# Kernel optimization log

Measured on AMD Instinct MI355X. Metric: run time of the kernel, lower is better.

The kernel has to match this reference:

```python
import jax
import jax.numpy as jnp
import numpy as np
from jax import lax

DELTA = float(np.exp(-2.0))  # rule-creation density threshold


def codebook_lamb(x):
    """Online growing RBF prototype codebook (ALMMo-style) for one layer.

    x: [N, M]. Returns lamb: [N] normalized density of each sample at its
    assigned rule. Faithful (corrected) semantics of Layer.__call__:
      - SEN = squared L2 norm per sample (over feature dim)
      - global mean / mean squared norm over the batch
      - sequential per-sample: if max RBF density over existing rules < exp(-2),
        append a new rule (prototype=c=x, SENc=||x||^2, support=1);
        else update rule_star. Note the source's `support[rule_star] = +1`
        assigns 1, so the running mean update degenerates to c[rule_star]=x,
        SENc[rule_star]=||x||^2 -- replicated here.
      - distances use the (never-updated) prototypes; bandwidth stau uses c.
    """
    N, M = x.shape
    SENx = jnp.sum(x * x, axis=-1)                      # [N]
    gmean = jnp.mean(x, axis=0)                         # [M]
    base = jnp.mean(SENx) - jnp.sum(gmean * gmean)      # SENgmean - SEN(gmean)
    R = N                                               # worst case: one rule/sample

    protos0 = jnp.zeros((R, M), x.dtype)
    pn20 = jnp.zeros((R,), x.dtype)                     # ||proto_r||^2 (carried)
    c0 = jnp.zeros((R, M), x.dtype)
    cn20 = jnp.zeros((R,), x.dtype)                     # ||c_r||^2 (carried)
    SENc0 = jnp.zeros((R,), x.dtype)
    count0 = jnp.int32(0)

    ridx = jnp.arange(R)

    def step(carry, inp):
        protos, pn2, c, cn2, SENc, count = carry
        xi, sxi = inp                                   # [M], scalar
        valid = ridx < count
        stau = (base + SENc - cn2) * 0.5                # [R]
        dist = sxi + pn2 - 2.0 * (protos @ xi)          # [R] ||xi - proto_r||^2
        dens = jnp.where(valid, jnp.exp(-dist / stau), -jnp.inf)
        idx = jnp.argmax(dens)
        vmax = dens[idx]
        new = (count == 0) | (vmax < DELTA)
        slot = jnp.where(new, count, idx)
        # both branches set c/SENc at slot to xi/sxi (support resets to 1)
        c = c.at[slot].set(xi)
        cn2 = cn2.at[slot].set(sxi)
        SENc = SENc.at[slot].set(sxi)
        # only a new rule writes a prototype (OOB scatter when count==R is dropped)
        protos = protos.at[count].set(jnp.where(new, xi, protos[count]))
        pn2 = pn2.at[count].set(jnp.where(new, sxi, pn2[count]))
        count = count + new.astype(count.dtype)
        return (protos, pn2, c, cn2, SENc, count), slot

    (protos, pn2, c, cn2, SENc, count), rules = lax.scan(
        step, (protos0, pn20, c0, cn20, SENc0, count0), (x, SENx)
    )

    # final densities of all samples under all (valid) rules: [R, N]
    stau = (base + SENc - cn2) * 0.5                    # [R]
    dist = SENx[None, :] + pn2[:, None] - 2.0 * (protos @ x.T)
    dens = jnp.where((ridx < count)[:, None], jnp.exp(-dist / stau[:, None]), 0.0)
    dens_xn = dens[rules, jnp.arange(N)]                # density at assigned rule
    lamb = dens_xn / jnp.sum(dens, axis=0)              # normalize over rules
    return lamb


def setup_inputs() -> dict:
    key = jax.random.key(0)
    k = jax.random.split(key, 5)
    N, D_IN, D_H, D_OUT = 2048, 2048, 2048, 1024
    s0 = 1.0 / np.sqrt(D_IN)
    s1 = 1.0 / np.sqrt(D_H)
    return {
        "x": jax.random.normal(k[0], (N, D_IN), jnp.float32),
        "W0": jax.random.normal(k[1], (D_H, D_IN), jnp.float32) * s0,
        "b0": jax.random.normal(k[2], (D_H,), jnp.float32) * s0,
        "W1": jax.random.normal(k[3], (D_OUT, D_H), jnp.float32) * s1,
        "b1": jax.random.normal(k[4], (D_OUT,), jnp.float32) * s1,
    }


def reference(x, W0, b0, W1, b1):
    lambs = []
    h = x
    for W, b in ((W0, b0), (W1, b1)):
        lambs.append(codebook_lamb(h))          # per-layer codebook on layer input
        h = jax.nn.sigmoid(h @ W.T + b)         # torch.nn.Linear + sigmoid
    return h, jnp.stack(lambs)                  # ([N, d_out], [n_layers, N])
```

## Files before the change

### kernel.cpp

```cpp
#include <hip/hip_runtime.h>
#include <cstdint>
#include <cstddef>


#define DELTA_F 0.13533528323661270f
#define MBYTE (1u << 20)

typedef __bf16 bf16;
typedef bf16 bf16x8 __attribute__((ext_vector_type(8)));
typedef bf16 bf16x4 __attribute__((ext_vector_type(4)));
typedef float f32x4 __attribute__((ext_vector_type(4)));

typedef __attribute__((address_space(1))) void as1_void;
typedef __attribute__((address_space(3))) void as3_void;

__device__ __forceinline__ void gload16(const bf16* g, bf16* l) {
  __builtin_amdgcn_global_load_lds((as1_void*)g, (as3_void*)l, 16, 0, 0);
}

template <bool IS_L0>
__global__ __launch_bounds__(512, 4) void gemm_fused(
    const bf16* __restrict__ A, float* __restrict__ Dens,
    bf16* __restrict__ Hb, float* __restrict__ Fo,
    const float* __restrict__ bias, const float* __restrict__ SENin,
    const float* __restrict__ ninv_p, float* __restrict__ S,
    int* __restrict__ e, float* __restrict__ SENhOut,
    float* __restrict__ colsumH) {
  __shared__ __align__(16) char smem[32768];
  const int tid = threadIdx.x;
  const int wave = tid >> 6, lane = tid & 63;
  const int quad = lane >> 4, l16 = lane & 15;
  const int kg = wave & 1, wm = (wave >> 1) & 1, wn = (wave >> 2) & 1;
  const int m0 = blockIdx.y * 128, n0 = blockIdx.x * 128;
  const int waveM = wm * 64, waveN = wn * 64;
  const bool isGram = (n0 < 2048);
  const int sr8 = lane >> 3, slot = lane & 7;
  const int gk = (slot ^ sr8) * 8;
  const bf16* aSrc = A + (size_t)(m0 + wave * 16 + sr8) * 2048 + gk;
  const bf16* bSrc = A + (size_t)(n0 + wave * 16 + sr8) * 2048 + gk;
  char* const aDst = smem + wave * 2048;
  char* const bDst = smem + 16384 + wave * 2048;
  const int swz = ((kg * 4 + quad) ^ (l16 & 7)) * 16;
  const int aOff = (waveM + l16) * 128 + swz;
  const int bOff = 16384 + (waveN + l16) * 128 + swz;

  f32x4 acc[4][4] = {};
  for (int k0 = 0; k0 < 2048; k0 += 64) {
    gload16(aSrc + k0, (bf16*)aDst);
    gload16(aSrc + 8 * 2048 + k0, (bf16*)(aDst + 1024));
    gload16(bSrc + k0, (bf16*)bDst);
    gload16(bSrc + 8 * 2048 + k0, (bf16*)(bDst + 1024));
    __syncthreads();
    bf16x8 af[4], bfr[4];
#pragma unroll
    for (int i = 0; i < 4; ++i) af[i] = *(const bf16x8*)(smem + aOff + i * 2048);
#pragma unroll
    for (int j = 0; j < 4; ++j) bfr[j] = *(const bf16x8*)(smem + bOff + j * 2048);
#pragma unroll
    for (int i = 0; i < 4; ++i)
#pragma unroll
      for (int j = 0; j < 4; ++j)
        acc[i][j] = __builtin_amdgcn_mfma_f32_16x16x32_bf16(af[i], bfr[j], acc[i][j], 0, 0, 0);
    __syncthreads();
  }

  const float ninv = ninv_p[0];
  float colp[4] = {0.f, 0.f, 0.f, 0.f};
  char* const ex = smem + (wn * 2 + wm) * 8192;
#pragma unroll
  for (int round = 0; round < 2; ++round) {
    __syncthreads();
    if (kg == 1) {
#pragma unroll
      for (int ii = 0; ii < 2; ++ii)
#pragma unroll
        for (int j = 0; j < 4; ++j)
          *(f32x4*)(ex + (ii * 4 + j) * 1024 + lane * 16) = acc[round * 2 + ii][j];
    }
    __syncthreads();
    if (kg == 0) {
#pragma unroll
      for (int ii = 0; ii < 2; ++ii) {
        const int i = round * 2 + ii;
        const int rbase = m0 + waveM + i * 16 + quad * 4;
        if (isGram) {
          const f32x4 si4 = *(const f32x4*)(SENin + rbase);
          float rp[4] = {0.f, 0.f, 0.f, 0.f};
          int er = 0;
#pragma unroll
          for (int j = 0; j < 4; ++j) {
            f32x4 v = acc[i][j] + *(const f32x4*)(ex + (ii * 4 + j) * 1024 + lane * 16);
            const int col = n0 + waveN + j * 16 + l16;
            const float sj = SENin[col];
#pragma unroll
            for (int r = 0; r < 4; ++r) {
              const float dens = __expf((si4[r] + sj - 2.0f * v[r]) * ninv);
              Dens[(size_t)(rbase + r) * 2048 + col] = dens;
              rp[r] += dens;
              if (col < rbase + r && dens >= DELTA_F) er |= (1 << r);
            }
          }
#pragma unroll
          for (int r = 0; r < 4; ++r) {
            float rv = rp[r];
            rv += __shfl_xor(rv, 1, 64); rv += __shfl_xor(rv, 2, 64);
            rv += __shfl_xor(rv, 4, 64); rv += __shfl_xor(rv, 8, 64);
            if (l16 == 0) atomicAdd(S + rbase + r, rv);
          }
          er |= __shfl_xor(er, 1, 64); er |= __shfl_xor(er, 2, 64);
          er |= __shfl_xor(er, 4, 64); er |= __shfl_xor(er, 8, 64);
          if (l16 == 0 && er) {
#pragma unroll
            for (int r = 0; r < 4; ++r)
              if ((er >> r) & 1) atomicOr(e + rbase + r, 1);
          }
        } else {
          float rn[4] = {0.f, 0.f, 0.f, 0.f};
#pragma unroll
          for (int j = 0; j < 4; ++j) {
            f32x4 v = acc[i][j] + *(const f32x4*)(ex + (ii * 4 + j) * 1024 + lane * 16);
            const int c2 = n0 - 2048 + waveN + j * 16 + l16;
            const float bv = bias[c2];
#pragma unroll
            for (int r = 0; r < 4; ++r) {
              const float hv = 1.0f / (1.0f + __expf(-(v[r] + bv)));
              if (IS_L0) {
                Hb[(size_t)(rbase + r) * 2048 + c2] = (bf16)hv;
                rn[r] += hv * hv;
                colp[j] += hv;
              } else {
                Fo[(size_t)(rbase + r) * 1024 + c2] = hv;
              }
            }
          }
          if (IS_L0) {
#pragma unroll
            for (int r = 0; r < 4; ++r) {
              float rv = rn[r];
              rv += __shfl_xor(rv, 1, 64); rv += __shfl_xor(rv, 2, 64);
              rv += __shfl_xor(rv, 4, 64); rv += __shfl_xor(rv, 8, 64);
              if (l16 == 0) atomicAdd(SENhOut + rbase + r, rv);
            }
          }
        }
      }
    }
  }
  if (IS_L0 && !isGram && kg == 0) {
#pragma unroll
    for (int j = 0; j < 4; ++j) {
      float cv = colp[j];
      cv += __shfl_xor(cv, 16, 64);
      cv += __shfl_xor(cv, 32, 64);
      if (lane < 16) atomicAdd(colsumH + (n0 - 2048 + waveN + j * 16 + lane), cv);
    }
  }
}

__device__ __forceinline__ float wave_reduce(float s) {
  for (int o = 32; o > 0; o >>= 1) s += __shfl_down(s, o, 64);
  return s;
}

__global__ void f2b_all(const float* __restrict__ x, const float* __restrict__ W0,
                        const float* __restrict__ W1, bf16* __restrict__ xb,
                        bf16* __restrict__ wb0, bf16* __restrict__ wb1,
                        float* __restrict__ SENx, float* __restrict__ cpartX) {
  const int b = blockIdx.x, tid = threadIdx.x;
  const int wave = tid >> 6, lane = tid & 63;
  if (b < 256) {
    const int r0 = b * 8;
    __shared__ float ws[8][4];
    f32x4 c0 = {0.f, 0.f, 0.f, 0.f}, c1 = {0.f, 0.f, 0.f, 0.f};
    for (int r = 0; r < 8; ++r) {
      const float* src = x + (size_t)(r0 + r) * 2048;
      bf16* dst = xb + (size_t)(r0 + r) * 2048;
      f32x4 v0 = *(const f32x4*)(src + tid * 4);
      f32x4 v1 = *(const f32x4*)(src + 1024 + tid * 4);
      bf16x4 o0, o1;
      o0.x = (bf16)v0.x; o0.y = (bf16)v0.y; o0.z = (bf16)v0.z; o0.w = (bf16)v0.w;
      o1.x = (bf16)v1.x; o1.y = (bf16)v1.y; o1.z = (bf16)v1.z; o1.w = (bf16)v1.w;
      *(bf16x4*)(dst + tid * 4) = o0;
      *(bf16x4*)(dst + 1024 + tid * 4) = o1;
      c0 += v0; c1 += v1;
      float rn = v0.x * v0.x + v0.y * v0.y + v0.z * v0.z + v0.w * v0.w +
                 v1.x * v1.x + v1.y * v1.y + v1.z * v1.z + v1.w * v1.w;
      rn = wave_reduce(rn);
      if (lane == 0) ws[r][wave] = rn;
    }
    __syncthreads();
    if (tid < 8) SENx[r0 + tid] = ws[tid][0] + ws[tid][1] + ws[tid][2] + ws[tid][3];
    float* bin = cpartX + (size_t)(b & 15) * 2048;
    atomicAdd(bin + tid * 4 + 0, c0.x); atomicAdd(bin + tid * 4 + 1, c0.y);
    atomicAdd(bin + tid * 4 + 2, c0.z); atomicAdd(bin + tid * 4 + 3, c0.w);
    atomicAdd(bin + 1024 + tid * 4 + 0, c1.x); atomicAdd(bin + 1024 + tid * 4 + 1, c1.y);
    atomicAdd(bin + 1024 + tid * 4 + 2, c1.z); atomicAdd(bin + 1024 + tid * 4 + 3, c1.w);
  } else if (b < 512) {
    const size_t base = (size_t)(b - 256) * 16384;
    for (int c = tid * 4; c < 16384; c += 1024) {
      f32x4 v = *(const f32x4*)(W0 + base + c);
      bf16x4 o;
      o.x = (bf16)v.x; o.y = (bf16)v.y; o.z = (bf16)v.z; o.w = (bf16)v.w;
      *(bf16x4*)(wb0 + base + c) = o;
    }
  } else {
    const size_t base = (size_t)(b - 512) * 16384;
    for (int c = tid * 4; c < 16384; c += 1024) {
      f32x4 v = *(const f32x4*)(W1 + base + c);
      bf16x4 o;
      o.x = (bf16)v.x; o.y = (bf16)v.y; o.z = (bf16)v.z; o.w = (bf16)v.w;
      *(bf16x4*)(wb1 + base + c) = o;
    }
  }
}

__global__ void stau0_kernel(const float* __restrict__ SENx,
                             const float* __restrict__ cpartX,
                             float* __restrict__ scal) {
  const int tid = threadIdx.x;
  float ssen = 0.f;
  for (int i = tid; i < 2048; i += 256) ssen += SENx[i];
  float sg2 = 0.f;
  for (int c = tid; c < 2048; c += 256) {
    float cs = 0.f;
#pragma unroll
    for (int p = 0; p < 16; ++p) cs += cpartX[(size_t)p * 2048 + c];
    const float gm = cs * (1.f / 2048.f);
    sg2 += gm * gm;
  }
  __shared__ float r1[256], r2[256];
  r1[tid] = ssen; r2[tid] = sg2;
  __syncthreads();
  for (int s = 128; s; s >>= 1) {
    if (tid < s) { r1[tid] += r1[tid + s]; r2[tid] += r2[tid + s]; }
    __syncthreads();
  }
  if (tid == 0) {
    const float stau = 0.5f * (r1[0] * (1.f / 2048.f) - r2[0]);
    scal[0] = stau;
    scal[1] = -1.f / stau;
  }
}

template <bool STAU1>
__global__ void decide_lamb(const int* __restrict__ e, const float* __restrict__ Dens,
                            const float* __restrict__ S, float* __restrict__ lamb,
                            const float* __restrict__ SENh,
                            const float* __restrict__ colsumH,
                            float* __restrict__ scalOut) {
  __shared__ char s_flag[2048];
  __shared__ short s_as[2048];
  __shared__ short s_list[2048];
  __shared__ short s_re[2048];
  __shared__ int scan_[256];
  __shared__ float rbest[256];
  __shared__ int rbj[256];
  __shared__ int s_T, s_reN;
  __shared__ float r1[256], r2[256];
  const int tid = threadIdx.x;

  if (STAU1) {
    float ssen = 0.f;
    for (int i = tid; i < 2048; i += 256) ssen += SENh[i];
    float sg2 = 0.f;
    for (int c = tid; c < 2048; c += 256) {
      const float gm = colsumH[c] * (1.f / 2048.f);
      sg2 += gm * gm;
    }
    r1[tid] = ssen; r2[tid] = sg2;
    __syncthreads();
    for (int s = 128; s; s >>= 1) {
      if (tid < s) { r1[tid] += r1[tid + s]; r2[tid] += r2[tid + s]; }
      __syncthreads();
    }
    if (tid == 0) {
      const float stau = 0.5f * (r1[0] * (1.f / 2048.f) - r2[0]);
      scalOut[4] = stau;
      scalOut[5] = -1.f / stau;
    }
    __syncthreads();
  }

  int cnt = 0;
#pragma unroll
  for (int k = 0; k < 8; ++k) {
    const int i = tid * 8 + k;
    const int ei = e[i];
    s_flag[i] = (ei == 0);
    if (ei == 0) s_as[i] = (short)i;
    cnt += ei;
  }
  scan_[tid] = cnt;
  if (tid == 0) s_reN = 0;
  __syncthreads();
  for (int off = 1; off < 256; off <<= 1) {
    const int v = scan_[tid];
    const int add = (tid >= off) ? scan_[tid - off] : 0;
    __syncthreads();
    scan_[tid] = v + add;
    __syncthreads();
  }
  int pos = scan_[tid] - cnt;
#pragma unroll
  for (int k = 0; k < 8; ++k) {
    const int i = tid * 8 + k;
    if (!s_flag[i]) s_list[pos++] = (short)i;
  }
  if (tid == 255) s_T = scan_[255];
  __syncthreads();
  const int T = s_T;
  for (int t = 0; t < T; ++t) {
    const int i = s_list[t];
    const float* di = Dens + (size_t)i * 2048;
    float best = -1.0f;
    int bestj = 0x7fffffff;
    for (int j = tid; j < i; j += 256) {
      if (s_flag[j]) {
        const float d = di[j];
        if (d > best || (d == best && j < bestj)) { best = d; bestj = j; }
      }
    }
    rbest[tid] = best; rbj[tid] = bestj;
    __syncthreads();
    if (tid == 0) {
      float b = -1.0f;
      int bj = 0x7fffffff;
      for (int k = 0; k < 256; ++k)
        if (rbest[k] > b || (rbest[k] == b && rbj[k] < bj)) { b = rbest[k]; bj = rbj[k]; }
      if (b < DELTA_F) { s_flag[i] = 1; s_as[i] = (short)i; }
      else { s_as[i] = (short)bj; s_re[s_reN++] = (short)i; }
    }
    __syncthreads();
  }
  const int reN = s_reN;
  for (int n = tid; n < 2048; n += 256) {
    const int aa = s_as[n];
    const float* dn = Dens + (size_t)n * 2048;
    float denom = S[n];
    for (int t = 0; t < reN; ++t) denom -= dn[s_re[t]];
    lamb[n] = dn[aa] / denom;
  }
}

extern "C" void kernel_launch(void* const* d_in, const int* in_sizes, int n_in,
                              void* d_out, int out_size, void* d_ws, size_t ws_size,
                              hipStream_t stream) {
  const float* x = (const float*)d_in[0];
  const float* W0 = (const float*)d_in[1];
  const float* b0 = (const float*)d_in[2];
  const float* W1 = (const float*)d_in[3];
  const float* b1 = (const float*)d_in[4];
  float* out = (float*)d_out;

  char* w = (char*)d_ws;
  bf16* xb = (bf16*)(w);
  bf16* wb0 = (bf16*)(w + 8 * MBYTE);
  bf16* hb = (bf16*)(w + 16 * MBYTE);
  bf16* wb1 = (bf16*)(w + 24 * MBYTE);
  float* Dens = (float*)(w + 28 * MBYTE);
  float* SENx = (float*)(w + 44 * MBYTE);
  float* scal = SENx + 2048;
  float* zbase = scal + 16;
  float* SENh = zbase;
  float* cpartX = SENh + 2048;
  float* colsumH = cpartX + 16 * 2048;
  float* S0 = colsumH + 2048;
  float* S1 = S0 + 2048;
  int* e0 = (int*)(S1 + 2048);
  int* e1 = e0 + 2048;
  const size_t zbytes = (size_t)(2048 * 7 + 16 * 2048) * 4;

  float* lamb0 = out + (size_t)2048 * 1024;
  float* lamb1 = lamb0 + 2048;

  hipMemsetAsync(zbase, 0, zbytes, stream);
  f2b_all<<<640, 256, 0, stream>>>(x, W0, W1, xb, wb0, wb1, SENx, cpartX);
  stau0_kernel<<<1, 256, 0, stream>>>(SENx, cpartX, scal);
  gemm_fused<true><<<dim3(32, 16), 512, 0, stream>>>(
      xb, Dens, hb, nullptr, b0, SENx, scal + 1, S0, e0, SENh, colsumH);
  decide_lamb<true><<<1, 256, 0, stream>>>(e0, Dens, S0, lamb0, SENh, colsumH, scal);
  gemm_fused<false><<<dim3(24, 16), 512, 0, stream>>>(
      hb, Dens, nullptr, out, b1, SENh, scal + 5, S1, e1, nullptr, nullptr);
  decide_lamb<false><<<1, 256, 0, stream>>>(e1, Dens, S1, lamb1, nullptr, nullptr, nullptr);
}
```

Before: 207.5 us.

## Fold decide/lambda pass into GEMM last-block tail and drop memset

The separate single-block decide_lamb kernels are removed. Their work now runs in the last-finishing block of each fused GEMM, detected with an atomic counter and threadfence, which saves two kernel launches. The hipMemsetAsync is replaced by zeroing inside f2b_all. The column-mean partials are written per block without atomics and reduced by an 8-block stau kernel that uses a last-block finalize. Diagonal densities are cached with atomicExch so the lambda numerator avoids a global re-read. The tail runs with 512 threads, but it is still serial, and the last-block pattern depends on correct memory fences.

```diff
diff --git a/kernel.cpp b/kernel.cpp
--- a/kernel.cpp
+++ b/kernel.cpp
@@ -5,6 +5,7 @@
 
 #define DELTA_F 0.13533528323661270f
 #define MBYTE (1u << 20)
+#define ZRE_WORDS 16400
 
 typedef __bf16 bf16;
 typedef bf16 bf16x8 __attribute__((ext_vector_type(8)));
@@ -16,6 +17,11 @@
 
 __device__ __forceinline__ void gload16(const bf16* g, bf16* l) {
   __builtin_amdgcn_global_load_lds((as1_void*)g, (as3_void*)l, 16, 0, 0);
+}
+
+__device__ __forceinline__ float wave_reduce(float s) {
+  for (int o = 32; o > 0; o >>= 1) s += __shfl_down(s, o, 64);
+  return s;
 }
 
 template <bool IS_L0>
@@ -25,8 +31,11 @@
     const float* __restrict__ bias, const float* __restrict__ SENin,
     const float* __restrict__ ninv_p, float* __restrict__ S,
     int* __restrict__ e, float* __restrict__ SENhOut,
-    float* __restrict__ colsumH) {
+    float* __restrict__ colsumH, float* __restrict__ diagD,
+    int* __restrict__ cnt, float* __restrict__ scalOut,
+    float* __restrict__ lambOut, int nblocks) {
   __shared__ __align__(16) char smem[32768];
+  __shared__ int s_last;
   const int tid = threadIdx.x;
   const int wave = tid >> 6, lane = tid & 63;
   const int quad = lane >> 4, l16 = lane & 15;
@@ -98,6 +107,7 @@
               Dens[(size_t)(rbase + r) * 2048 + col] = dens;
               rp[r] += dens;
               if (col < rbase + r && dens >= DELTA_F) er |= (1 << r);
+              if (col == rbase + r) atomicExch(diagD + col, dens);
             }
           }
 #pragma unroll
@@ -155,17 +165,119 @@
       if (lane < 16) atomicAdd(colsumH + (n0 - 2048 + waveN + j * 16 + lane), cv);
     }
   }
-}
-
-__device__ __forceinline__ float wave_reduce(float s) {
-  for (int o = 32; o > 0; o >>= 1) s += __shfl_down(s, o, 64);
-  return s;
+
+  __syncthreads();
+  if (tid == 0) {
+    __threadfence();
+    s_last = (atomicAdd(cnt, 1) == nblocks - 1);
+  }
+  __syncthreads();
+  if (!s_last) return;
+  __threadfence();
+
+  char* s_flag = smem;
+  short* s_as = (short*)(smem + 2048);
+  short* s_list = (short*)(smem + 6144);
+  short* s_re = (short*)(smem + 10240);
+  int* scan_ = (int*)(smem + 14336);
+  float* rbest = (float*)(smem + 16384);
+  int* rbj = (int*)(smem + 18432);
+  float* r1 = (float*)(smem + 20480);
+  float* r2 = (float*)(smem + 22528);
+  int* sT = (int*)(smem + 24576);
+  int* sReN = (int*)(smem + 24580);
+
+  if (IS_L0) {
+    float ssen = 0.f, sg2 = 0.f;
+    for (int i = tid; i < 2048; i += 512) ssen += atomicAdd(SENhOut + i, 0.f);
+    for (int c = tid; c < 2048; c += 512) {
+      const float gm = atomicAdd(colsumH + c, 0.f) * (1.f / 2048.f);
+      sg2 += gm * gm;
+    }
+    r1[tid] = ssen; r2[tid] = sg2;
+    __syncthreads();
+    for (int s = 256; s; s >>= 1) {
+      if (tid < s) { r1[tid] += r1[tid + s]; r2[tid] += r2[tid + s]; }
+      __syncthreads();
+    }
+    if (tid == 0) {
+      const float stau = 0.5f * (r1[0] * (1.f / 2048.f) - r2[0]);
+      scalOut[4] = stau;
+      scalOut[5] = -1.f / stau;
+    }
+    __syncthreads();
+  }
+
+  int cntl = 0;
+#pragma unroll
+  for (int k = 0; k < 4; ++k) {
+    const int i = tid * 4 + k;
+    const int ei = atomicOr(e + i, 0);
+    s_flag[i] = (ei == 0);
+    if (ei == 0) s_as[i] = (short)i;
+    cntl += (ei != 0);
+  }
+  scan_[tid] = cntl;
+  if (tid == 0) sReN[0] = 0;
+  __syncthreads();
+  for (int off = 1; off < 512; off <<= 1) {
+    const int v = scan_[tid];
+    const int add = (tid >= off) ? scan_[tid - off] : 0;
+    __syncthreads();
+    scan_[tid] = v + add;
+    __syncthreads();
+  }
+  int pos = scan_[tid] - cntl;
+#pragma unroll
+  for (int k = 0; k < 4; ++k) {
+    const int i = tid * 4 + k;
+    if (!s_flag[i]) s_list[pos++] = (short)i;
+  }
+  if (tid == 511) sT[0] = scan_[511];
+  __syncthreads();
+  const int T = sT[0];
+  for (int t = 0; t < T; ++t) {
+    const int i = s_list[t];
+    const float* di = Dens + (size_t)i * 2048;
+    float best = -1.0f;
+    int bestj = 0x7fffffff;
+    for (int j = tid; j < i; j += 512) {
+      if (s_flag[j]) {
+        const float d = di[j];
+        if (d > best || (d == best && j < bestj)) { best = d; bestj = j; }
+      }
+    }
+    rbest[tid] = best; rbj[tid] = bestj;
+    __syncthreads();
+    if (tid == 0) {
+      float b = -1.0f;
+      int bj = 0x7fffffff;
+      for (int k = 0; k < 512; ++k)
+        if (rbest[k] > b || (rbest[k] == b && rbj[k] < bj)) { b = rbest[k]; bj = rbj[k]; }
+      if (b < DELTA_F) { s_flag[i] = 1; s_as[i] = (short)i; }
+      else { s_as[i] = (short)bj; s_re[sReN[0]++] = (short)i; }
+    }
+    __syncthreads();
+  }
+  const int reN = sReN[0];
+
+#pragma unroll
+  for (int k = 0; k < 4; ++k) {
+    const int n = k * 512 + tid;
+    const int aa = s_as[n];
+    const float num = (aa == n) ? atomicAdd(diagD + n, 0.f)
+                                : Dens[(size_t)n * 2048 + aa];
+    float denom = atomicAdd(S + n, 0.f);
+    for (int t = 0; t < reN; ++t) denom -= Dens[(size_t)n * 2048 + s_re[t]];
+    lambOut[n] = num / denom;
+  }
 }
 
 __global__ void f2b_all(const float* __restrict__ x, const float* __restrict__ W0,
                         const float* __restrict__ W1, bf16* __restrict__ xb,
                         bf16* __restrict__ wb0, bf16* __restrict__ wb1,
-                        float* __restrict__ SENx, float* __restrict__ cpartX) {
+                        float* __restrict__ SENx, float* __restrict__ cpart,
+                        int* __restrict__ zre) {
   const int b = blockIdx.x, tid = threadIdx.x;
   const int wave = tid >> 6, lane = tid & 63;
   if (b < 256) {
@@ -190,11 +302,9 @@
     }
     __syncthreads();
     if (tid < 8) SENx[r0 + tid] = ws[tid][0] + ws[tid][1] + ws[tid][2] + ws[tid][3];
-    float* bin = cpartX + (size_t)(b & 15) * 2048;
-    atomicAdd(bin + tid * 4 + 0, c0.x); atomicAdd(bin + tid * 4 + 1, c0.y);
-    atomicAdd(bin + tid * 4 + 2, c0.z); atomicAdd(bin + tid * 4 + 3, c0.w);
-    atomicAdd(bin + 1024 + tid * 4 + 0, c1.x); atomicAdd(bin + 1024 + tid * 4 + 1, c1.y);
-    atomicAdd(bin + 1024 + tid * 4 + 2, c1.z); atomicAdd(bin + 1024 + tid * 4 + 3, c1.w);
+    float* bin = cpart + (size_t)b * 2048;
+    *(f32x4*)(bin + tid * 4) = c0;
+    *(f32x4*)(bin + 1024 + tid * 4) = c1;
   } else if (b < 512) {
     const size_t base = (size_t)(b - 256) * 16384;
     for (int c = tid * 4; c < 16384; c += 1024) {
@@ -211,134 +321,45 @@
       o.x = (bf16)v.x; o.y = (bf16)v.y; o.z = (bf16)v.z; o.w = (bf16)v.w;
       *(bf16x4*)(wb1 + base + c) = o;
     }
+    const int idx = (b - 512) * 256 + tid;
+    if (idx < ZRE_WORDS) zre[idx] = 0;
   }
 }
 
 __global__ void stau0_kernel(const float* __restrict__ SENx,
-                             const float* __restrict__ cpartX,
-                             float* __restrict__ scal) {
-  const int tid = threadIdx.x;
+                             const float* __restrict__ cpart,
+                             float* __restrict__ accS, float* __restrict__ accG,
+                             int* __restrict__ cntS, float* __restrict__ scal) {
+  const int p = blockIdx.x, tid = threadIdx.x;
+  const int col = p * 256 + tid;
+  float s = 0.f;
+  for (int r = 0; r < 256; ++r) s += cpart[(size_t)r * 2048 + col];
+  const float gm = s * (1.f / 2048.f);
+  float sg2 = gm * gm;
   float ssen = 0.f;
-  for (int i = tid; i < 2048; i += 256) ssen += SENx[i];
-  float sg2 = 0.f;
-  for (int c = tid; c < 2048; c += 256) {
-    float cs = 0.f;
-#pragma unroll
-    for (int p = 0; p < 16; ++p) cs += cpartX[(size_t)p * 2048 + c];
-    const float gm = cs * (1.f / 2048.f);
-    sg2 += gm * gm;
-  }
+  if (p == 0)
+    for (int i = tid; i < 2048; i += 256) ssen += SENx[i];
   __shared__ float r1[256], r2[256];
-  r1[tid] = ssen; r2[tid] = sg2;
-  __syncthreads();
-  for (int s = 128; s; s >>= 1) {
-    if (tid < s) { r1[tid] += r1[tid + s]; r2[tid] += r2[tid + s]; }
+  __shared__ int s_last;
+  r1[tid] = sg2; r2[tid] = ssen;
+  __syncthreads();
+  for (int st = 128; st; st >>= 1) {
+    if (tid < st) { r1[tid] += r1[tid + st]; r2[tid] += r2[tid + st]; }
     __syncthreads();
   }
   if (tid == 0) {
-    const float stau = 0.5f * (r1[0] * (1.f / 2048.f) - r2[0]);
+    atomicAdd(accG, r1[0]);
+    if (p == 0) atomicAdd(accS, r2[0]);
+    __threadfence();
+    s_last = (atomicAdd(cntS, 1) == 7);
+  }
+  __syncthreads();
+  if (tid == 0 && s_last) {
+    const float vG = atomicAdd(accG, 0.f);
+    const float vS = atomicAdd(accS, 0.f);
+    const float stau = 0.5f * (vS * (1.f / 2048.f) - vG);
     scal[0] = stau;
     scal[1] = -1.f / stau;
-  }
-}
-
-template <bool STAU1>
-__global__ void decide_lamb(const int* __restrict__ e, const float* __restrict__ Dens,
-                            const float* __restrict__ S, float* __restrict__ lamb,
-                            const float* __restrict__ SENh,
-                            const float* __restrict__ colsumH,
-                            float* __restrict__ scalOut) {
-  __shared__ char s_flag[2048];
-  __shared__ short s_as[2048];
-  __shared__ short s_list[2048];
-  __shared__ short s_re[2048];
-  __shared__ int scan_[256];
-  __shared__ float rbest[256];
-  __shared__ int rbj[256];
-  __shared__ int s_T, s_reN;
-  __shared__ float r1[256], r2[256];
-  const int tid = threadIdx.x;
-
-  if (STAU1) {
-    float ssen = 0.f;
-    for (int i = tid; i < 2048; i += 256) ssen += SENh[i];
-    float sg2 = 0.f;
-    for (int c = tid; c < 2048; c += 256) {
-      const float gm = colsumH[c] * (1.f / 2048.f);
-      sg2 += gm * gm;
-    }
-    r1[tid] = ssen; r2[tid] = sg2;
-    __syncthreads();
-    for (int s = 128; s; s >>= 1) {
-      if (tid < s) { r1[tid] += r1[tid + s]; r2[tid] += r2[tid + s]; }
-      __syncthreads();
-    }
-    if (tid == 0) {
-      const float stau = 0.5f * (r1[0] * (1.f / 2048.f) - r2[0]);
-      scalOut[4] = stau;
-      scalOut[5] = -1.f / stau;
-    }
-    __syncthreads();
-  }
-
-  int cnt = 0;
-#pragma unroll
-  for (int k = 0; k < 8; ++k) {
-    const int i = tid * 8 + k;
-    const int ei = e[i];
-    s_flag[i] = (ei == 0);
-    if (ei == 0) s_as[i] = (short)i;
-    cnt += ei;
-  }
-  scan_[tid] = cnt;
-  if (tid == 0) s_reN = 0;
-  __syncthreads();
-  for (int off = 1; off < 256; off <<= 1) {
-    const int v = scan_[tid];
-    const int add = (tid >= off) ? scan_[tid - off] : 0;
-    __syncthreads();
-    scan_[tid] = v + add;
-    __syncthreads();
-  }
-  int pos = scan_[tid] - cnt;
-#pragma unroll
-  for (int k = 0; k < 8; ++k) {
-    const int i = tid * 8 + k;
-    if (!s_flag[i]) s_list[pos++] = (short)i;
-  }
-  if (tid == 255) s_T = scan_[255];
-  __syncthreads();
-  const int T = s_T;
-  for (int t = 0; t < T; ++t) {
-    const int i = s_list[t];
-    const float* di = Dens + (size_t)i * 2048;
-    float best = -1.0f;
-    int bestj = 0x7fffffff;
-    for (int j = tid; j < i; j += 256) {
-      if (s_flag[j]) {
-        const float d = di[j];
-        if (d > best || (d == best && j < bestj)) { best = d; bestj = j; }
-      }
-    }
-    rbest[tid] = best; rbj[tid] = bestj;
-    __syncthreads();
-    if (tid == 0) {
-      float b = -1.0f;
-      int bj = 0x7fffffff;
-      for (int k = 0; k < 256; ++k)
-        if (rbest[k] > b || (rbest[k] == b && rbj[k] < bj)) { b = rbest[k]; bj = rbj[k]; }
-      if (b < DELTA_F) { s_flag[i] = 1; s_as[i] = (short)i; }
-      else { s_as[i] = (short)bj; s_re[s_reN++] = (short)i; }
-    }
-    __syncthreads();
-  }
-  const int reN = s_reN;
-  for (int n = tid; n < 2048; n += 256) {
-    const int aa = s_as[n];
-    const float* dn = Dens + (size_t)n * 2048;
-    float denom = S[n];
-    for (int t = 0; t < reN; ++t) denom -= dn[s_re[t]];
-    lamb[n] = dn[aa] / denom;
   }
 }
 
@@ -359,27 +380,32 @@
   bf16* wb1 = (bf16*)(w + 24 * MBYTE);
   float* Dens = (float*)(w + 28 * MBYTE);
   float* SENx = (float*)(w + 44 * MBYTE);
-  float* scal = SENx + 2048;
-  float* zbase = scal + 16;
-  float* SENh = zbase;
-  float* cpartX = SENh + 2048;
-  float* colsumH = cpartX + 16 * 2048;
+  float* cpart = SENx + 2048;
+  float* scal = cpart + 256 * 2048;
+  float* zre = scal + 16;
+  float* SENh = zre;
+  float* colsumH = SENh + 2048;
   float* S0 = colsumH + 2048;
   float* S1 = S0 + 2048;
-  int* e0 = (int*)(S1 + 2048);
+  float* diagD0 = S1 + 2048;
+  float* diagD1 = diagD0 + 2048;
+  int* e0 = (int*)(diagD1 + 2048);
   int* e1 = e0 + 2048;
-  const size_t zbytes = (size_t)(2048 * 7 + 16 * 2048) * 4;
+  float* accS = (float*)(e1 + 2048);
+  float* accG = accS + 1;
+  int* cntS = (int*)(accG + 1);
+  int* cnt0 = cntS + 1;
+  int* cnt1 = cnt0 + 1;
 
   float* lamb0 = out + (size_t)2048 * 1024;
   float* lamb1 = lamb0 + 2048;
 
-  hipMemsetAsync(zbase, 0, zbytes, stream);
-  f2b_all<<<640, 256, 0, stream>>>(x, W0, W1, xb, wb0, wb1, SENx, cpartX);
-  stau0_kernel<<<1, 256, 0, stream>>>(SENx, cpartX, scal);
+  f2b_all<<<640, 256, 0, stream>>>(x, W0, W1, xb, wb0, wb1, SENx, cpart, (int*)zre);
+  stau0_kernel<<<8, 256, 0, stream>>>(SENx, cpart, accS, accG, cntS, scal);
   gemm_fused<true><<<dim3(32, 16), 512, 0, stream>>>(
-      xb, Dens, hb, nullptr, b0, SENx, scal + 1, S0, e0, SENh, colsumH);
-  decide_lamb<true><<<1, 256, 0, stream>>>(e0, Dens, S0, lamb0, SENh, colsumH, scal);
+      xb, Dens, hb, nullptr, b0, SENx, scal + 1, S0, e0, SENh, colsumH,
+      diagD0, cnt0, scal, lamb0, 512);
   gemm_fused<false><<<dim3(24, 16), 512, 0, stream>>>(
-      hb, Dens, nullptr, out, b1, SENh, scal + 5, S1, e1, nullptr, nullptr);
-  decide_lamb<false><<<1, 256, 0, stream>>>(e1, Dens, S1, lamb1, nullptr, nullptr, nullptr);
-}
+      hb, Dens, nullptr, out, b1, SENh, scal + 5, S1, e1, nullptr, nullptr,
+      diagD1, cnt1, nullptr, lamb1, 384);
+}
```

After: 229.9 us. 10.8% more time.
